# Performance work log

Hardware: AMD Instinct MI355X
Metric: run time of the kernel (lower is better)

The kernel has to match this reference:

```python
import jax, jax.numpy as jnp
import numpy as np

B, L, D, T = 32, 512, 1024, 256
MAX_MENTION_LEN = 10
NEG_INF = float('-inf')


def _static_bounds_and_keep():
    # Full (start, end) grid, flattened row-major like torch's .view(-1, 2)
    s = np.repeat(np.arange(L), L)
    e = np.tile(np.arange(L), L)
    bounds = np.stack([s, e], axis=-1)            # [L*L, 2]
    keep = (e - s) <= MAX_MENTION_LEN             # static per-position mask
    idx = np.nonzero(keep)[0]
    return jnp.asarray(bounds[keep], jnp.int32), jnp.asarray(idx, jnp.int32)


def setup_inputs() -> dict:
    key = jax.random.key(0)
    k0, k1, k2 = jax.random.split(key, 3)
    text_encodings = jax.random.normal(k0, (B, L, D), dtype=jnp.float32)
    mask_ctxt = jnp.ones((B, L), dtype=jnp.int32)
    # word -> wordpiece mapping: [start, end_exclusive); values kept in [1, L)
    tokens_mapping = jax.random.randint(k1, (B, T, 2), 1, L).astype(jnp.int32)
    W = jax.random.normal(k2, (D, 3), dtype=jnp.float32) * 0.02
    b = jnp.zeros((3,), dtype=jnp.float32)
    return {"text_encodings": text_encodings, "mask_ctxt": mask_ctxt,
            "tokens_mapping": tokens_mapping, "W": W, "b": b}


def reference(text_encodings, mask_ctxt, tokens_mapping, W, b):
    # per-token start / end / mention logits
    logits = jnp.einsum('bld,dk->blk', text_encodings, W) + b  # [B, L, 3]
    valid_tok = (mask_ctxt == 1)
    start_lp = jnp.where(valid_tok, logits[:, :, 0], NEG_INF)
    end_lp = jnp.where(valid_tok, logits[:, :, 1], NEG_INF)
    mention_lp = jnp.where(valid_tok, logits[:, :, 2], NEG_INF)

    # scores[b, s, e] = start[b, s] + end[b, e] + sum_{i=s..e} mention[b, i]
    scores = start_lp[:, :, None] + end_lp[:, None, :]          # [B, L, L]
    csum = jnp.cumsum(mention_lp, axis=1)                        # [B, L]
    csum_prev = jnp.concatenate(
        [jnp.zeros((csum.shape[0], 1), csum.dtype), csum[:, :-1]], axis=1)
    scores = scores + (csum[:, None, :] - csum_prev[:, :, None])

    # mention_sizes > 0  <=>  e >= s
    pos = jnp.arange(L)
    size_ok = pos[None, :, None] <= pos[None, None, :]           # [1, L, L]

    # token-boundary masks (scatter 1 at word starts / ends, zero col 0)
    bidx = jnp.arange(tokens_mapping.shape[0])[:, None]
    ts = jnp.zeros(mask_ctxt.shape, jnp.int32).at[bidx, tokens_mapping[:, :, 0]].set(1)
    ts = ts.at[:, 0].set(0)
    te = jnp.zeros(mask_ctxt.shape, jnp.int32).at[bidx, tokens_mapping[:, :, 1] - 1].set(1)
    te = te.at[:, 0].set(0)
    vse = ts[:, :, None] * te[:, None, :]                        # bmm outer product

    valid = size_ok & (mask_ctxt[:, :, None] > 0) & (vse > 0)
    scores = jnp.where(valid, scores, NEG_INF)

    scores_flat = scores.reshape(scores.shape[0], -1)            # [B, L*L]
    bounds_keep, keep_idx = _static_bounds_and_keep()
    out_scores = scores_flat[:, keep_idx]                        # [B, K]
    out_bounds = jnp.broadcast_to(bounds_keep[None],
                                  (scores.shape[0],) + bounds_keep.shape)
    return out_scores, out_bounds
```

## Files before the change

kernel.cpp:

```cpp
#include <hip/hip_runtime.h>
#include <math.h>

#define BB 32
#define LL 512
#define DD 1024
#define TT 256
#define NK 136393
#define NK_LIN 131273
#define S_LIN 502
#define NEG_BIG  -3.0e38f
#define NEG_MASK -1.0e30f

__global__ __launch_bounds__(256) void logits_kernel(
    const float* __restrict__ text, const float* __restrict__ W,
    const float* __restrict__ bias, const int* __restrict__ mask,
    const int* __restrict__ tmap,
    float* __restrict__ slp, float* __restrict__ elp, float* __restrict__ mlp,
    int* __restrict__ fs, int* __restrict__ fe)
{
    __shared__ int tsl[LL];
    __shared__ int tel[LL];
    const int wid  = threadIdx.x >> 6;
    const int lane = threadIdx.x & 63;
    const int row  = blockIdx.x * 4 + wid;
    const int b    = blockIdx.x;
    const int t    = threadIdx.x;

    if (b < BB) {
        tsl[t] = 0; tsl[t + 256] = 0;
        tel[t] = 0; tel[t + 256] = 0;
        __syncthreads();
        int s0 = tmap[((size_t)b * TT + t) * 2 + 0];
        int e0 = tmap[((size_t)b * TT + t) * 2 + 1] - 1;
        s0 = min(max(s0, 0), LL - 1);
        e0 = min(max(e0, 0), LL - 1);
        tsl[s0] = 1;
        tel[e0] = 1;
        __syncthreads();
    }

    const float4* t4 = (const float4*)(text + (size_t)row * DD);
    float a0 = 0.f, a1 = 0.f, a2 = 0.f;
#pragma unroll
    for (int j = 0; j < 4; ++j) {
        const int fi = lane + j * 64;
        float4 v = t4[fi];
        const float* wp = W + (size_t)fi * 12;
        a0 += v.x * wp[0];  a1 += v.x * wp[1];  a2 += v.x * wp[2];
        a0 += v.y * wp[3];  a1 += v.y * wp[4];  a2 += v.y * wp[5];
        a0 += v.z * wp[6];  a1 += v.z * wp[7];  a2 += v.z * wp[8];
        a0 += v.w * wp[9];  a1 += v.w * wp[10]; a2 += v.w * wp[11];
    }
#pragma unroll
    for (int off = 32; off; off >>= 1) {
        a0 += __shfl_down(a0, off);
        a1 += __shfl_down(a1, off);
        a2 += __shfl_down(a2, off);
    }
    if (lane == 0) {
        const int m = mask[row];
        slp[row] = (m == 1) ? a0 + bias[0] : NEG_MASK;
        elp[row] = (m == 1) ? a1 + bias[1] : NEG_MASK;
        mlp[row] = (m == 1) ? a2 + bias[2] : NEG_MASK;
    }

    if (b < BB) {
        const int i0 = b * LL + t, i1 = i0 + 256;
        fs[i0] = (t != 0 && mask[i0] == 1 && tsl[t]) ? 1 : 0;
        fs[i1] = (mask[i1] == 1 && tsl[t + 256]) ? 1 : 0;
        fe[i0] = (t != 0 && tel[t]) ? 1 : 0;
        fe[i1] = tel[t + 256] ? 1 : 0;
    }
}

__global__ __launch_bounds__(256) void out_kernel(
    const float* __restrict__ slp, const float* __restrict__ elp,
    const float* __restrict__ mlp,
    const int* __restrict__ fs, const int* __restrict__ fe,
    float* __restrict__ out)
{
    const int k = blockIdx.x * 256 + threadIdx.x;
    const int b = blockIdx.y;
    if (k >= NK) return;

    int s, e;
    if (k >= NK_LIN) {
        const int r = k - NK_LIN;
        s = S_LIN + (r >> 9);
        e = r & 511;
    } else {
        float f = sqrtf(8.0f * (float)k + 441.0f);
        s = (int)((f - 21.0f) * 0.5f);
        if (s < 0) s = 0;
        if (s > 501) s = 501;
        while ((s + 1) * (s + 22) / 2 <= k) ++s;
        while (s * (s + 21) / 2 > k) --s;
        e = k - s * (s + 21) / 2;
    }

    const int base = b * LL;
    float score = NEG_BIG;
    if (s <= e && fs[base + s] && fe[base + e]) {
        float w = 0.f;
        for (int l = s; l <= e; ++l) w += mlp[base + l];
        score = (slp[base + s] + elp[base + e]) + w;
    }

    out[(size_t)b * NK + k] = score;

    float2* bptr = (float2*)(out + (size_t)BB * NK);
    bptr[(size_t)b * NK + k] = make_float2((float)s, (float)e);
}

extern "C" void kernel_launch(void* const* d_in, const int* in_sizes, int n_in,
                              void* d_out, int out_size, void* d_ws, size_t ws_size,
                              hipStream_t stream) {
    const float* text = (const float*)d_in[0];
    const int*   mask = (const int*)d_in[1];
    const int*   tmap = (const int*)d_in[2];
    const float* W    = (const float*)d_in[3];
    const float* bias = (const float*)d_in[4];
    float* out = (float*)d_out;

    float* slp = (float*)d_ws;
    float* elp = slp + (size_t)BB * LL;
    float* mlp = elp + (size_t)BB * LL;
    int*   fs  = (int*)(mlp + (size_t)BB * LL);
    int*   fe  = fs + (size_t)BB * LL;

    logits_kernel<<<BB * LL / 4, 256, 0, stream>>>(text, W, bias, mask, tmap,
                                                   slp, elp, mlp, fs, fe);
    dim3 g3((NK + 255) / 256, BB);
    out_kernel<<<g3, 256, 0, stream>>>(slp, elp, mlp, fs, fe, out);
}
```

Before: 31.82 us.

## Map output kernel to one block per start row, add nontemporal loads/stores

```diff
diff --git a/kernel.cpp b/kernel.cpp
--- a/kernel.cpp
+++ b/kernel.cpp
@@ -10,6 +10,9 @@
 #define S_LIN 502
 #define NEG_BIG  -3.0e38f
 #define NEG_MASK -1.0e30f
+
+typedef float f4v __attribute__((ext_vector_type(4)));
+typedef float f2v __attribute__((ext_vector_type(2)));
 
 __global__ __launch_bounds__(256) void logits_kernel(
     const float* __restrict__ text, const float* __restrict__ W,
@@ -39,17 +42,20 @@
         __syncthreads();
     }
 
-    const float4* t4 = (const float4*)(text + (size_t)row * DD);
+    const f4v* t4 = (const f4v*)(text + (size_t)row * DD);
+    const f4v* w4 = (const f4v*)W;
     float a0 = 0.f, a1 = 0.f, a2 = 0.f;
 #pragma unroll
     for (int j = 0; j < 4; ++j) {
         const int fi = lane + j * 64;
-        float4 v = t4[fi];
-        const float* wp = W + (size_t)fi * 12;
-        a0 += v.x * wp[0];  a1 += v.x * wp[1];  a2 += v.x * wp[2];
-        a0 += v.y * wp[3];  a1 += v.y * wp[4];  a2 += v.y * wp[5];
-        a0 += v.z * wp[6];  a1 += v.z * wp[7];  a2 += v.z * wp[8];
-        a0 += v.w * wp[9];  a1 += v.w * wp[10]; a2 += v.w * wp[11];
+        f4v v  = __builtin_nontemporal_load(&t4[fi]);
+        f4v w0 = w4[fi * 3 + 0];
+        f4v w1 = w4[fi * 3 + 1];
+        f4v w2 = w4[fi * 3 + 2];
+        a0 += v.x * w0.x;  a1 += v.x * w0.y;  a2 += v.x * w0.z;
+        a0 += v.y * w0.w;  a1 += v.y * w1.x;  a2 += v.y * w1.y;
+        a0 += v.z * w1.z;  a1 += v.z * w1.w;  a2 += v.z * w2.x;
+        a0 += v.w * w2.y;  a1 += v.w * w2.z;  a2 += v.w * w2.w;
     }
 #pragma unroll
     for (int off = 32; off; off >>= 1) {
@@ -79,37 +85,32 @@
     const int* __restrict__ fs, const int* __restrict__ fe,
     float* __restrict__ out)
 {
-    const int k = blockIdx.x * 256 + threadIdx.x;
+    const int s = blockIdx.x;
     const int b = blockIdx.y;
-    if (k >= NK) return;
+    const int t = threadIdx.x;
+    const int rowlen = min(LL, s + 11);
+    const size_t obase = (size_t)b * NK +
+        (s <= S_LIN ? s * (s + 21) / 2 : NK_LIN + (s - S_LIN) * LL);
+    const int base = b * LL;
+    const int   fss = fs[base + s];
+    const float sv  = slp[base + s];
+    f2v* bptr = (f2v*)(out + (size_t)BB * NK);
 
-    int s, e;
-    if (k >= NK_LIN) {
-        const int r = k - NK_LIN;
-        s = S_LIN + (r >> 9);
-        e = r & 511;
-    } else {
-        float f = sqrtf(8.0f * (float)k + 441.0f);
-        s = (int)((f - 21.0f) * 0.5f);
-        if (s < 0) s = 0;
-        if (s > 501) s = 501;
-        while ((s + 1) * (s + 22) / 2 <= k) ++s;
-        while (s * (s + 21) / 2 > k) --s;
-        e = k - s * (s + 21) / 2;
+#pragma unroll
+    for (int h = 0; h < 2; ++h) {
+        const int e = t + h * 256;
+        if (e < rowlen) {
+            float score = NEG_BIG;
+            if (e >= s && fss && fe[base + e]) {
+                float w = 0.f;
+                for (int l = s; l <= e; ++l) w += mlp[base + l];
+                score = (sv + elp[base + e]) + w;
+            }
+            __builtin_nontemporal_store(score, &out[obase + e]);
+            f2v bv; bv.x = (float)s; bv.y = (float)e;
+            __builtin_nontemporal_store(bv, &bptr[obase + e]);
+        }
     }
-
-    const int base = b * LL;
-    float score = NEG_BIG;
-    if (s <= e && fs[base + s] && fe[base + e]) {
-        float w = 0.f;
-        for (int l = s; l <= e; ++l) w += mlp[base + l];
-        score = (slp[base + s] + elp[base + e]) + w;
-    }
-
-    out[(size_t)b * NK + k] = score;
-
-    float2* bptr = (float2*)(out + (size_t)BB * NK);
-    bptr[(size_t)b * NK + k] = make_float2((float)s, (float)e);
 }
 
 extern "C" void kernel_launch(void* const* d_in, const int* in_sizes, int n_in,
@@ -130,6 +131,6 @@
 
     logits_kernel<<<BB * LL / 4, 256, 0, stream>>>(text, W, bias, mask, tmap,
                                                    slp, elp, mlp, fs, fe);
-    dim3 g3((NK + 255) / 256, BB);
-    out_kernel<<<g3, 256, 0, stream>>>(slp, elp, mlp, fs, fe, out);
+    dim3 g2(LL, BB);
+    out_kernel<<<g2, 256, 0, stream>>>(slp, elp, mlp, fs, fe, out);
 }
```

Measured after the change: 32.34 us. About the same (+1.6%).
